# Kernel tuning notes

Measured on AMD Instinct MI355X. Metric: run time of the kernel, lower is better.

The kernel has to match this reference:

```python
import jax, jax.numpy as jnp
import numpy as np

N_CLASSES = 16384
M = 2
D = 128


def setup_inputs() -> dict:
    key = jax.random.key(0)
    k1, k2 = jax.random.split(key)
    x = jax.random.normal(k1, (N_CLASSES * M, D), dtype=jnp.float32)
    anchor_idx = jax.random.randint(k2, (N_CLASSES,), 0, M, dtype=jnp.int64 if jax.config.jax_enable_x64 else jnp.int32).astype(jnp.int32)
    pos_idx = (1 - anchor_idx).astype(jnp.int32)  # randperm(2) -> positive is the other sample
    return {"x": x, "anchor_idx": anchor_idx, "pos_idx": pos_idx}


def reference(x, anchor_idx, pos_idx):
    # x: [N*M, D]; anchor_idx/pos_idx: [N] in [0, M)
    N = anchor_idx.shape[0]
    Dx = x.shape[1]
    xr = x.reshape(N, M, Dx)
    anchors = jnp.take_along_axis(xr, anchor_idx[:, None, None], axis=1)[:, 0, :]    # [N, D]
    positives = jnp.take_along_axis(xr, pos_idx[:, None, None], axis=1)[:, 0, :]     # [N, D]
    negs = xr[:, 1, :]                                                               # [N, D] (sample 1 of every class)
    # score[i, j] = a_i . (neg_j - pos_i) = a_i . neg_j - a_i . pos_i
    S = anchors @ negs.T                                                             # [N, N]
    ap = jnp.sum(anchors * positives, axis=1)                                        # [N]
    logits = S - ap[:, None]
    mask = ~jnp.eye(N, dtype=bool)                                                   # exclude j == i (own class)
    sums = jnp.sum(jnp.where(mask, jnp.exp(logits), jnp.float32(0.0)), axis=1)       # [N]
    return jnp.sum(jnp.log1p(sums))
```

## Files before the change

### kernel.cpp

```cpp
#include <hip/hip_runtime.h>
#include <hip/hip_bf16.h>
#include <math.h>

#define N_CLS 16384
#define DDIM  128
#define LOG2E 1.4426950408889634f

#if __has_builtin(__builtin_amdgcn_exp2f)
#define EXP2(x) __builtin_amdgcn_exp2f(x)
#else
#define EXP2(x) exp2f(x)
#endif

typedef __attribute__((ext_vector_type(8))) short short8;
typedef __attribute__((ext_vector_type(16))) float f32x16;

__device__ __forceinline__ unsigned short f2bf(float f) {
    __hip_bfloat16 h = __float2bfloat16(f);
    return *(unsigned short*)&h;
}

__global__ __launch_bounds__(256)
void prep_kernel(const float* __restrict__ x,
                 const int* __restrict__ aidx,
                 float* __restrict__ ap,
                 unsigned short* __restrict__ Afrag,
                 unsigned short* __restrict__ Bfrag,
                 float* __restrict__ out) {
    const int t = threadIdx.x;
    const int g = blockIdx.x;
    #pragma unroll
    for (int u = 0; u < 4; ++u) {
        const int l  = u * 256 + t;
        const int r  = l >> 4;
        const int k0 = (l & 15) * 8;
        const float* src = x + (long)g * 8192 + (long)r * 128 + k0;
        float fa[8];
        *(float4*)&fa[0] = *(const float4*)(src);
        *(float4*)&fa[4] = *(const float4*)(src + 4);
        const long dst = (long)g * 4096 +
                         ((l & 15) >> 1) * 512 + ((l & 1) * 32 + (r >> 1)) * 8;
        if (r & 1) {
            short8 B;
            #pragma unroll
            for (int j = 0; j < 8; ++j) B[j] = (short)f2bf(fa[j]);
            *(short8*)(Bfrag + dst) = B;
        } else {
            float fb[8];
            *(float4*)&fb[0] = *(const float4*)(src + 128);
            *(float4*)&fb[4] = *(const float4*)(src + 132);
            const int i = g * 32 + (r >> 1);
            const bool sel = (aidx[i] != 0);
            short8 A;
            float d = 0.0f;
            #pragma unroll
            for (int j = 0; j < 8; ++j) {
                const float av = sel ? fb[j] : fa[j];
                A[j] = (short)f2bf(av * LOG2E);
                d += fa[j] * fb[j];
            }
            *(short8*)(Afrag + dst) = A;
            d += __shfl_xor(d, 1, 64);
            d += __shfl_xor(d, 2, 64);
            d += __shfl_xor(d, 4, 64);
            d += __shfl_xor(d, 8, 64);
            if ((t & 15) == 0) ap[i] = d;
        }
    }
    if (t == 0 && g == 0) out[0] = 0.0f;
}

__global__ __launch_bounds__(256, 3)
void fused_kernel(const unsigned short* __restrict__ Afrag,
                  const unsigned short* __restrict__ Bfrag,
                  float* __restrict__ partial) {
    __shared__ __align__(16) unsigned short bs[2][4096];
    const int tid  = threadIdx.x;
    const int lane = tid & 63;
    const int w    = tid >> 6;
    const int l31  = lane & 31;
    const int hi   = lane >> 5;
    const int oct  = blockIdx.x & 7;
    const int rt   = blockIdx.x >> 3;
    const int r0   = rt * 8 + w * 2;
    const int r1   = r0 + 1;

    short8 af0[8], af1[8];
    {
        const unsigned short* a0 = Afrag + (long)r0 * 4096 + lane * 8;
        const unsigned short* a1 = Afrag + (long)r1 * 4096 + lane * 8;
        #pragma unroll
        for (int kc = 0; kc < 8; ++kc) {
            af0[kc] = *(const short8*)(a0 + kc * 512);
            af1[kc] = *(const short8*)(a1 + kc * 512);
        }
    }
    const unsigned short* bbase = Bfrag + (long)oct * (64L * 4096) + lane * 8;
    const int wchunk = w * 1024;

    const int ctd0 = r0 - oct * 64;
    const int ctd1 = r1 - oct * 64;

    float rs0[16], rs1[16];
    #pragma unroll
    for (int q = 0; q < 16; ++q) { rs0[q] = 0.0f; rs1[q] = 0.0f; }

    {
        short8 s0 = *(const short8*)(bbase + wchunk);
        short8 s1 = *(const short8*)(bbase + wchunk + 512);
        *(short8*)(&bs[0][wchunk + lane * 8]) = s0;
        *(short8*)(&bs[0][wchunk + 512 + lane * 8]) = s1;
    }
    __syncthreads();

    for (int ct = 0; ct < 64; ++ct) {
        const int cur = ct & 1;
        const long nt = (ct < 63) ? (long)(ct + 1) : 63L;
        short8 n0 = *(const short8*)(bbase + nt * 4096 + wchunk);
        short8 n1 = *(const short8*)(bbase + nt * 4096 + wchunk + 512);

        f32x16 acc0, acc1;
        #pragma unroll
        for (int q = 0; q < 16; ++q) { acc0[q] = 0.0f; acc1[q] = 0.0f; }

        const unsigned short* bp = &bs[cur][lane * 8];
        #pragma unroll
        for (int kc = 0; kc < 8; ++kc) {
            short8 b = *(const short8*)(bp + kc * 512);
            acc0 = __builtin_amdgcn_mfma_f32_32x32x16_bf16(af0[kc], b, acc0, 0, 0, 0);
            acc1 = __builtin_amdgcn_mfma_f32_32x32x16_bf16(af1[kc], b, acc1, 0, 0, 0);
        }

        if (ct == ctd0) {
            #pragma unroll
            for (int q = 0; q < 16; ++q) {
                const float e = EXP2(acc0[q]);
                const int row = (q & 3) + 8 * (q >> 2) + 4 * hi;
                rs0[q] += (l31 == row) ? 0.0f : e;
            }
        } else {
            #pragma unroll
            for (int q = 0; q < 16; ++q) rs0[q] += EXP2(acc0[q]);
        }
        if (ct == ctd1) {
            #pragma unroll
            for (int q = 0; q < 16; ++q) {
                const float e = EXP2(acc1[q]);
                const int row = (q & 3) + 8 * (q >> 2) + 4 * hi;
                rs1[q] += (l31 == row) ? 0.0f : e;
            }
        } else {
            #pragma unroll
            for (int q = 0; q < 16; ++q) rs1[q] += EXP2(acc1[q]);
        }

        *(short8*)(&bs[cur ^ 1][wchunk + lane * 8]) = n0;
        *(short8*)(&bs[cur ^ 1][wchunk + 512 + lane * 8]) = n1;
        __syncthreads();
    }

    #pragma unroll
    for (int q = 0; q < 16; ++q) {
        float v0 = rs0[q], v1 = rs1[q];
        v0 += __shfl_xor(v0, 1, 64);  v1 += __shfl_xor(v1, 1, 64);
        v0 += __shfl_xor(v0, 2, 64);  v1 += __shfl_xor(v1, 2, 64);
        v0 += __shfl_xor(v0, 4, 64);  v1 += __shfl_xor(v1, 4, 64);
        v0 += __shfl_xor(v0, 8, 64);  v1 += __shfl_xor(v1, 8, 64);
        v0 += __shfl_xor(v0, 16, 64); v1 += __shfl_xor(v1, 16, 64);
        if (l31 == 0) {
            const int row = (q & 3) + 8 * (q >> 2) + 4 * hi;
            partial[(long)oct * N_CLS + (long)r0 * 32 + row] = v0;
            partial[(long)oct * N_CLS + (long)r1 * 32 + row] = v1;
        }
    }
}

__global__ __launch_bounds__(256)
void finalize_kernel(const float* __restrict__ partial,
                     const float* __restrict__ ap,
                     float* __restrict__ out) {
    __shared__ float red[256];
    const int t = threadIdx.x;
    const int row = blockIdx.x * 256 + t;
    float s = 0.0f;
    #pragma unroll
    for (int p = 0; p < 8; ++p) s += partial[(long)p * N_CLS + row];
    const float u = logf(s) - ap[row];
    const float loss = (u > 25.0f) ? u : log1pf(__expf(u));
    red[t] = loss;
    __syncthreads();
    for (int st = 128; st > 0; st >>= 1) {
        if (t < st) red[t] += red[t + st];
        __syncthreads();
    }
    if (t == 0) atomicAdd(out, red[0]);
}

extern "C" void kernel_launch(void* const* d_in, const int* in_sizes, int n_in,
                              void* d_out, int out_size, void* d_ws, size_t ws_size,
                              hipStream_t stream) {
    const float* x    = (const float*)d_in[0];
    const int*   aidx = (const int*)d_in[1];

    char* ws = (char*)d_ws;
    float* ap             = (float*)(ws);
    float* partial        = (float*)(ws + 131072);
    unsigned short* Afrag = (unsigned short*)(ws + 131072 + 1048576);
    unsigned short* Bfrag = (unsigned short*)(ws + 131072 + 1048576 + 4194304);

    prep_kernel<<<N_CLS / 32, 256, 0, stream>>>(x, aidx, ap, Afrag, Bfrag, (float*)d_out);
    fused_kernel<<<512, 256, 0, stream>>>(Afrag, Bfrag, partial);
    finalize_kernel<<<64, 256, 0, stream>>>(partial, ap, (float*)d_out);
}
```

Before: 141.1 us.

## Software-pipeline MFMA and exp epilogue across double accumulator sets

Splits the column-tile loop into compute and epilogue stages with two sets of accumulators, so the exp2/row-sum epilogue of tile t-1 is issued while the MFMAs for tile t run. The goal is to overlap the transcendental VALU work with matrix-core latency instead of serializing them. The extra accumulators raise register pressure, so launch bounds drop from 3 to 2 waves-per-SIMD occupancy, which could reduce latency hiding elsewhere.

```diff
diff --git a/kernel.cpp b/kernel.cpp
--- a/kernel.cpp
+++ b/kernel.cpp
@@ -70,7 +70,7 @@
     if (t == 0 && g == 0) out[0] = 0.0f;
 }
 
-__global__ __launch_bounds__(256, 3)
+__global__ __launch_bounds__(256, 2)
 void fused_kernel(const unsigned short* __restrict__ Afrag,
                   const unsigned short* __restrict__ Bfrag,
                   float* __restrict__ partial) {
@@ -98,12 +98,65 @@
     const unsigned short* bbase = Bfrag + (long)oct * (64L * 4096) + lane * 8;
     const int wchunk = w * 1024;
 
-    const int ctd0 = r0 - oct * 64;
-    const int ctd1 = r1 - oct * 64;
+    int ctd0 = r0 - oct * 64;
+    int ctd1 = r1 - oct * 64;
+    if (ctd0 < 0 || ctd0 >= 64) ctd0 = -1000;
+    if (ctd1 < 0 || ctd1 >= 64) ctd1 = -1000;
 
     float rs0[16], rs1[16];
     #pragma unroll
     for (int q = 0; q < 16; ++q) { rs0[q] = 0.0f; rs1[q] = 0.0f; }
+
+    const f32x16 zacc = {0.0f, 0.0f, 0.0f, 0.0f, 0.0f, 0.0f, 0.0f, 0.0f,
+                         0.0f, 0.0f, 0.0f, 0.0f, 0.0f, 0.0f, 0.0f, 0.0f};
+    f32x16 aA0, aA1, aB0, aB1;
+
+    auto compute = [&](f32x16& c0, f32x16& c1, const unsigned short* bp) {
+        #pragma unroll
+        for (int kc = 0; kc < 8; ++kc) {
+            short8 b = *(const short8*)(bp + kc * 512);
+            c0 = __builtin_amdgcn_mfma_f32_32x32x16_bf16(
+                     af0[kc], b, (kc == 0) ? zacc : c0, 0, 0, 0);
+            c1 = __builtin_amdgcn_mfma_f32_32x32x16_bf16(
+                     af1[kc], b, (kc == 0) ? zacc : c1, 0, 0, 0);
+        }
+    };
+    auto epi = [&](f32x16& p0, f32x16& p1, int pt) {
+        if (pt == ctd0) {
+            #pragma unroll
+            for (int q = 0; q < 16; ++q) {
+                const float e = EXP2(p0[q]);
+                const int row = (q & 3) + 8 * (q >> 2) + 4 * hi;
+                rs0[q] += (l31 == row) ? 0.0f : e;
+            }
+        } else {
+            #pragma unroll
+            for (int q = 0; q < 16; ++q) rs0[q] += EXP2(p0[q]);
+        }
+        if (pt == ctd1) {
+            #pragma unroll
+            for (int q = 0; q < 16; ++q) {
+                const float e = EXP2(p1[q]);
+                const int row = (q & 3) + 8 * (q >> 2) + 4 * hi;
+                rs1[q] += (l31 == row) ? 0.0f : e;
+            }
+        } else {
+            #pragma unroll
+            for (int q = 0; q < 16; ++q) rs1[q] += EXP2(p1[q]);
+        }
+    };
+    auto step = [&](int t, f32x16& c0, f32x16& c1,
+                    f32x16& p0, f32x16& p1, int pt) {
+        const int cur = t & 1;
+        const long nt = (t < 63) ? (long)(t + 1) : 63L;
+        short8 n0 = *(const short8*)(bbase + nt * 4096 + wchunk);
+        short8 n1 = *(const short8*)(bbase + nt * 4096 + wchunk + 512);
+        compute(c0, c1, &bs[cur][lane * 8]);
+        if (pt >= 0) epi(p0, p1, pt);
+        *(short8*)(&bs[cur ^ 1][wchunk + lane * 8]) = n0;
+        *(short8*)(&bs[cur ^ 1][wchunk + 512 + lane * 8]) = n1;
+        __syncthreads();
+    };
 
     {
         short8 s0 = *(const short8*)(bbase + wchunk);
@@ -113,51 +166,11 @@
     }
     __syncthreads();
 
-    for (int ct = 0; ct < 64; ++ct) {
-        const int cur = ct & 1;
-        const long nt = (ct < 63) ? (long)(ct + 1) : 63L;
-        short8 n0 = *(const short8*)(bbase + nt * 4096 + wchunk);
-        short8 n1 = *(const short8*)(bbase + nt * 4096 + wchunk + 512);
-
-        f32x16 acc0, acc1;
-        #pragma unroll
-        for (int q = 0; q < 16; ++q) { acc0[q] = 0.0f; acc1[q] = 0.0f; }
-
-        const unsigned short* bp = &bs[cur][lane * 8];
-        #pragma unroll
-        for (int kc = 0; kc < 8; ++kc) {
-            short8 b = *(const short8*)(bp + kc * 512);
-            acc0 = __builtin_amdgcn_mfma_f32_32x32x16_bf16(af0[kc], b, acc0, 0, 0, 0);
-            acc1 = __builtin_amdgcn_mfma_f32_32x32x16_bf16(af1[kc], b, acc1, 0, 0, 0);
-        }
-
-        if (ct == ctd0) {
-            #pragma unroll
-            for (int q = 0; q < 16; ++q) {
-                const float e = EXP2(acc0[q]);
-                const int row = (q & 3) + 8 * (q >> 2) + 4 * hi;
-                rs0[q] += (l31 == row) ? 0.0f : e;
-            }
-        } else {
-            #pragma unroll
-            for (int q = 0; q < 16; ++q) rs0[q] += EXP2(acc0[q]);
-        }
-        if (ct == ctd1) {
-            #pragma unroll
-            for (int q = 0; q < 16; ++q) {
-                const float e = EXP2(acc1[q]);
-                const int row = (q & 3) + 8 * (q >> 2) + 4 * hi;
-                rs1[q] += (l31 == row) ? 0.0f : e;
-            }
-        } else {
-            #pragma unroll
-            for (int q = 0; q < 16; ++q) rs1[q] += EXP2(acc1[q]);
-        }
-
-        *(short8*)(&bs[cur ^ 1][wchunk + lane * 8]) = n0;
-        *(short8*)(&bs[cur ^ 1][wchunk + 512 + lane * 8]) = n1;
-        __syncthreads();
-    }
+    for (int t = 0; t < 64; t += 2) {
+        step(t,     aA0, aA1, aB0, aB1, t - 1);
+        step(t + 1, aB0, aB1, aA0, aA1, t);
+    }
+    epi(aB0, aB1, 63);
 
     #pragma unroll
     for (int q = 0; q < 16; ++q) {
```

New measurement: 143.8 us. Within noise of the previous version (+1.9%).

## Halve per-wave row tiles in fused kernel, doubling grid and occupancy

Applied to the files above, without the earlier changes.

Each wave of the fused kernel now computes one 32-row anchor tile instead of two. The grid doubles to 1024 blocks and launch bounds rise to 4 blocks per SM, trading B-tile reuse for fewer registers and more parallelism. The MFMA loop is wrapped in s_setprio, and the prep kernel is flattened to one thread per 8-element slice that writes A and B fragments together. The cost is that B is loaded from global and LDS twice as often per unit of work.

```diff
diff --git a/kernel.cpp b/kernel.cpp
--- a/kernel.cpp
+++ b/kernel.cpp
@@ -27,50 +27,42 @@
                  unsigned short* __restrict__ Afrag,
                  unsigned short* __restrict__ Bfrag,
                  float* __restrict__ out) {
-    const int t = threadIdx.x;
-    const int g = blockIdx.x;
+    const int u  = blockIdx.x * 256 + threadIdx.x;
+    const int i  = u >> 4;
+    const int sl = u & 15;
+    const int k0 = sl * 8;
+
+    const float* pa = x + (2L * i) * DDIM + k0;
+    float fa[8], fb[8];
+    *(float4*)&fa[0] = *(const float4*)(pa);
+    *(float4*)&fa[4] = *(const float4*)(pa + 4);
+    *(float4*)&fb[0] = *(const float4*)(pa + DDIM);
+    *(float4*)&fb[4] = *(const float4*)(pa + DDIM + 4);
+    const bool sel = (aidx[i] != 0);
+
+    short8 A, B;
+    float d = 0.0f;
     #pragma unroll
-    for (int u = 0; u < 4; ++u) {
-        const int l  = u * 256 + t;
-        const int r  = l >> 4;
-        const int k0 = (l & 15) * 8;
-        const float* src = x + (long)g * 8192 + (long)r * 128 + k0;
-        float fa[8];
-        *(float4*)&fa[0] = *(const float4*)(src);
-        *(float4*)&fa[4] = *(const float4*)(src + 4);
-        const long dst = (long)g * 4096 +
-                         ((l & 15) >> 1) * 512 + ((l & 1) * 32 + (r >> 1)) * 8;
-        if (r & 1) {
-            short8 B;
-            #pragma unroll
-            for (int j = 0; j < 8; ++j) B[j] = (short)f2bf(fa[j]);
-            *(short8*)(Bfrag + dst) = B;
-        } else {
-            float fb[8];
-            *(float4*)&fb[0] = *(const float4*)(src + 128);
-            *(float4*)&fb[4] = *(const float4*)(src + 132);
-            const int i = g * 32 + (r >> 1);
-            const bool sel = (aidx[i] != 0);
-            short8 A;
-            float d = 0.0f;
-            #pragma unroll
-            for (int j = 0; j < 8; ++j) {
-                const float av = sel ? fb[j] : fa[j];
-                A[j] = (short)f2bf(av * LOG2E);
-                d += fa[j] * fb[j];
-            }
-            *(short8*)(Afrag + dst) = A;
-            d += __shfl_xor(d, 1, 64);
-            d += __shfl_xor(d, 2, 64);
-            d += __shfl_xor(d, 4, 64);
-            d += __shfl_xor(d, 8, 64);
-            if ((t & 15) == 0) ap[i] = d;
-        }
+    for (int j = 0; j < 8; ++j) {
+        const float av = sel ? fb[j] : fa[j];
+        A[j] = (short)f2bf(av * LOG2E);
+        B[j] = (short)f2bf(fb[j]);
+        d += fa[j] * fb[j];
     }
-    if (t == 0 && g == 0) out[0] = 0.0f;
+    const long dst = (long)(i >> 5) * 4096 + (sl >> 1) * 512 +
+                     ((sl & 1) * 32 + (i & 31)) * 8;
+    *(short8*)(Afrag + dst) = A;
+    *(short8*)(Bfrag + dst) = B;
+
+    d += __shfl_xor(d, 1, 64);
+    d += __shfl_xor(d, 2, 64);
+    d += __shfl_xor(d, 4, 64);
+    d += __shfl_xor(d, 8, 64);
+    if (sl == 0) ap[i] = d;
+    if (u == 0) out[0] = 0.0f;
 }
 
-__global__ __launch_bounds__(256, 3)
+__global__ __launch_bounds__(256, 4)
 void fused_kernel(const unsigned short* __restrict__ Afrag,
                   const unsigned short* __restrict__ Bfrag,
                   float* __restrict__ partial) {
@@ -82,28 +74,24 @@
     const int hi   = lane >> 5;
     const int oct  = blockIdx.x & 7;
     const int rt   = blockIdx.x >> 3;
-    const int r0   = rt * 8 + w * 2;
-    const int r1   = r0 + 1;
+    const int gRow = rt * 4 + w;
 
-    short8 af0[8], af1[8];
+    short8 af[8];
     {
-        const unsigned short* a0 = Afrag + (long)r0 * 4096 + lane * 8;
-        const unsigned short* a1 = Afrag + (long)r1 * 4096 + lane * 8;
+        const unsigned short* a0 = Afrag + (long)gRow * 4096 + lane * 8;
         #pragma unroll
-        for (int kc = 0; kc < 8; ++kc) {
-            af0[kc] = *(const short8*)(a0 + kc * 512);
-            af1[kc] = *(const short8*)(a1 + kc * 512);
-        }
+        for (int kc = 0; kc < 8; ++kc)
+            af[kc] = *(const short8*)(a0 + kc * 512);
     }
     const unsigned short* bbase = Bfrag + (long)oct * (64L * 4096) + lane * 8;
     const int wchunk = w * 1024;
 
-    const int ctd0 = r0 - oct * 64;
-    const int ctd1 = r1 - oct * 64;
+    int ctd = gRow - oct * 64;
+    if (ctd < 0 || ctd >= 64) ctd = -1000;
 
-    float rs0[16], rs1[16];
+    float rs[16];
     #pragma unroll
-    for (int q = 0; q < 16; ++q) { rs0[q] = 0.0f; rs1[q] = 0.0f; }
+    for (int q = 0; q < 16; ++q) rs[q] = 0.0f;
 
     {
         short8 s0 = *(const short8*)(bbase + wchunk);
@@ -119,39 +107,29 @@
         short8 n0 = *(const short8*)(bbase + nt * 4096 + wchunk);
         short8 n1 = *(const short8*)(bbase + nt * 4096 + wchunk + 512);
 
-        f32x16 acc0, acc1;
+        f32x16 acc;
         #pragma unroll
-        for (int q = 0; q < 16; ++q) { acc0[q] = 0.0f; acc1[q] = 0.0f; }
+        for (int q = 0; q < 16; ++q) acc[q] = 0.0f;
 
         const unsigned short* bp = &bs[cur][lane * 8];
+        __builtin_amdgcn_s_setprio(1);
         #pragma unroll
         for (int kc = 0; kc < 8; ++kc) {
             short8 b = *(const short8*)(bp + kc * 512);
-            acc0 = __builtin_amdgcn_mfma_f32_32x32x16_bf16(af0[kc], b, acc0, 0, 0, 0);
-            acc1 = __builtin_amdgcn_mfma_f32_32x32x16_bf16(af1[kc], b, acc1, 0, 0, 0);
+            acc = __builtin_amdgcn_mfma_f32_32x32x16_bf16(af[kc], b, acc, 0, 0, 0);
         }
+        __builtin_amdgcn_s_setprio(0);
 
-        if (ct == ctd0) {
+        if (ct == ctd) {
             #pragma unroll
             for (int q = 0; q < 16; ++q) {
-                const float e = EXP2(acc0[q]);
+                const float e = EXP2(acc[q]);
                 const int row = (q & 3) + 8 * (q >> 2) + 4 * hi;
-                rs0[q] += (l31 == row) ? 0.0f : e;
+                rs[q] += (l31 == row) ? 0.0f : e;
             }
         } else {
             #pragma unroll
-            for (int q = 0; q < 16; ++q) rs0[q] += EXP2(acc0[q]);
-        }
-        if (ct == ctd1) {
-            #pragma unroll
-            for (int q = 0; q < 16; ++q) {
-                const float e = EXP2(acc1[q]);
-                const int row = (q & 3) + 8 * (q >> 2) + 4 * hi;
-                rs1[q] += (l31 == row) ? 0.0f : e;
-            }
-        } else {
-            #pragma unroll
-            for (int q = 0; q < 16; ++q) rs1[q] += EXP2(acc1[q]);
+            for (int q = 0; q < 16; ++q) rs[q] += EXP2(acc[q]);
         }
 
         *(short8*)(&bs[cur ^ 1][wchunk + lane * 8]) = n0;
@@ -161,16 +139,15 @@
 
     #pragma unroll
     for (int q = 0; q < 16; ++q) {
-        float v0 = rs0[q], v1 = rs1[q];
-        v0 += __shfl_xor(v0, 1, 64);  v1 += __shfl_xor(v1, 1, 64);
-        v0 += __shfl_xor(v0, 2, 64);  v1 += __shfl_xor(v1, 2, 64);
-        v0 += __shfl_xor(v0, 4, 64);  v1 += __shfl_xor(v1, 4, 64);
-        v0 += __shfl_xor(v0, 8, 64);  v1 += __shfl_xor(v1, 8, 64);
-        v0 += __shfl_xor(v0, 16, 64); v1 += __shfl_xor(v1, 16, 64);
+        float v = rs[q];
+        v += __shfl_xor(v, 1, 64);
+        v += __shfl_xor(v, 2, 64);
+        v += __shfl_xor(v, 4, 64);
+        v += __shfl_xor(v, 8, 64);
+        v += __shfl_xor(v, 16, 64);
         if (l31 == 0) {
             const int row = (q & 3) + 8 * (q >> 2) + 4 * hi;
-            partial[(long)oct * N_CLS + (long)r0 * 32 + row] = v0;
-            partial[(long)oct * N_CLS + (long)r1 * 32 + row] = v1;
+            partial[(long)oct * N_CLS + (long)gRow * 32 + row] = v;
         }
     }
 }
@@ -208,7 +185,7 @@
     unsigned short* Afrag = (unsigned short*)(ws + 131072 + 1048576);
     unsigned short* Bfrag = (unsigned short*)(ws + 131072 + 1048576 + 4194304);
 
-    prep_kernel<<<N_CLS / 32, 256, 0, stream>>>(x, aidx, ap, Afrag, Bfrag, (float*)d_out);
-    fused_kernel<<<512, 256, 0, stream>>>(Afrag, Bfrag, partial);
+    prep_kernel<<<1024, 256, 0, stream>>>(x, aidx, ap, Afrag, Bfrag, (float*)d_out);
+    fused_kernel<<<1024, 256, 0, stream>>>(Afrag, Bfrag, partial);
     finalize_kernel<<<64, 256, 0, stream>>>(partial, ap, (float*)d_out);
 }
```

Result: slower. 143.9 us (+2.0%).

## Split column range into 16 groups, simplify prep, raise MFMA priority

Applied to the files above, without the earlier changes.

The fused kernel now splits the negative columns into 16 groups of 32 tiles instead of 8 groups of 64, launching 1024 blocks instead of 512. This gives more parallelism and better load balance across the CUs, at the cost of twice as many partial sums for finalize to read and twice the A-fragment reloads. The prep kernel is rewritten so each thread handles one 8-element slice of both samples of a class, producing the A and B fragments together. The MFMA loop is also wrapped in s_setprio to favour the matrix issue.

```diff
diff --git a/kernel.cpp b/kernel.cpp
--- a/kernel.cpp
+++ b/kernel.cpp
@@ -27,47 +27,39 @@
                  unsigned short* __restrict__ Afrag,
                  unsigned short* __restrict__ Bfrag,
                  float* __restrict__ out) {
-    const int t = threadIdx.x;
-    const int g = blockIdx.x;
-    #pragma unroll
-    for (int u = 0; u < 4; ++u) {
-        const int l  = u * 256 + t;
-        const int r  = l >> 4;
-        const int k0 = (l & 15) * 8;
-        const float* src = x + (long)g * 8192 + (long)r * 128 + k0;
-        float fa[8];
-        *(float4*)&fa[0] = *(const float4*)(src);
-        *(float4*)&fa[4] = *(const float4*)(src + 4);
-        const long dst = (long)g * 4096 +
-                         ((l & 15) >> 1) * 512 + ((l & 1) * 32 + (r >> 1)) * 8;
-        if (r & 1) {
-            short8 B;
-            #pragma unroll
-            for (int j = 0; j < 8; ++j) B[j] = (short)f2bf(fa[j]);
-            *(short8*)(Bfrag + dst) = B;
-        } else {
-            float fb[8];
-            *(float4*)&fb[0] = *(const float4*)(src + 128);
-            *(float4*)&fb[4] = *(const float4*)(src + 132);
-            const int i = g * 32 + (r >> 1);
-            const bool sel = (aidx[i] != 0);
-            short8 A;
-            float d = 0.0f;
-            #pragma unroll
-            for (int j = 0; j < 8; ++j) {
-                const float av = sel ? fb[j] : fa[j];
-                A[j] = (short)f2bf(av * LOG2E);
-                d += fa[j] * fb[j];
-            }
-            *(short8*)(Afrag + dst) = A;
-            d += __shfl_xor(d, 1, 64);
-            d += __shfl_xor(d, 2, 64);
-            d += __shfl_xor(d, 4, 64);
-            d += __shfl_xor(d, 8, 64);
-            if ((t & 15) == 0) ap[i] = d;
-        }
-    }
-    if (t == 0 && g == 0) out[0] = 0.0f;
+    const int u  = blockIdx.x * 256 + threadIdx.x;
+    const int i  = u >> 4;
+    const int sl = u & 15;
+    const int k0 = sl * 8;
+
+    const float* pa = x + (2L * i) * DDIM + k0;
+    float fa[8], fb[8];
+    *(float4*)&fa[0] = *(const float4*)(pa);
+    *(float4*)&fa[4] = *(const float4*)(pa + 4);
+    *(float4*)&fb[0] = *(const float4*)(pa + DDIM);
+    *(float4*)&fb[4] = *(const float4*)(pa + DDIM + 4);
+    const bool sel = (aidx[i] != 0);
+
+    short8 A, B;
+    float d = 0.0f;
+    #pragma unroll
+    for (int j = 0; j < 8; ++j) {
+        const float av = sel ? fb[j] : fa[j];
+        A[j] = (short)f2bf(av * LOG2E);
+        B[j] = (short)f2bf(fb[j]);
+        d += fa[j] * fb[j];
+    }
+    const long dst = (long)(i >> 5) * 4096 + (sl >> 1) * 512 +
+                     ((sl & 1) * 32 + (i & 31)) * 8;
+    *(short8*)(Afrag + dst) = A;
+    *(short8*)(Bfrag + dst) = B;
+
+    d += __shfl_xor(d, 1, 64);
+    d += __shfl_xor(d, 2, 64);
+    d += __shfl_xor(d, 4, 64);
+    d += __shfl_xor(d, 8, 64);
+    if (sl == 0) ap[i] = d;
+    if (u == 0) out[0] = 0.0f;
 }
 
 __global__ __launch_bounds__(256, 3)
@@ -80,8 +72,8 @@
     const int w    = tid >> 6;
     const int l31  = lane & 31;
     const int hi   = lane >> 5;
-    const int oct  = blockIdx.x & 7;
-    const int rt   = blockIdx.x >> 3;
+    const int cg   = blockIdx.x & 15;
+    const int rt   = blockIdx.x >> 4;
     const int r0   = rt * 8 + w * 2;
     const int r1   = r0 + 1;
 
@@ -95,11 +87,13 @@
             af1[kc] = *(const short8*)(a1 + kc * 512);
         }
     }
-    const unsigned short* bbase = Bfrag + (long)oct * (64L * 4096) + lane * 8;
+    const unsigned short* bbase = Bfrag + (long)cg * (32L * 4096) + lane * 8;
     const int wchunk = w * 1024;
 
-    const int ctd0 = r0 - oct * 64;
-    const int ctd1 = r1 - oct * 64;
+    int ctd0 = r0 - cg * 32;
+    int ctd1 = r1 - cg * 32;
+    if (ctd0 < 0 || ctd0 >= 32) ctd0 = -1000;
+    if (ctd1 < 0 || ctd1 >= 32) ctd1 = -1000;
 
     float rs0[16], rs1[16];
     #pragma unroll
@@ -113,9 +107,9 @@
     }
     __syncthreads();
 
-    for (int ct = 0; ct < 64; ++ct) {
+    for (int ct = 0; ct < 32; ++ct) {
         const int cur = ct & 1;
-        const long nt = (ct < 63) ? (long)(ct + 1) : 63L;
+        const long nt = (ct < 31) ? (long)(ct + 1) : 31L;
         short8 n0 = *(const short8*)(bbase + nt * 4096 + wchunk);
         short8 n1 = *(const short8*)(bbase + nt * 4096 + wchunk + 512);
 
@@ -124,12 +118,14 @@
         for (int q = 0; q < 16; ++q) { acc0[q] = 0.0f; acc1[q] = 0.0f; }
 
         const unsigned short* bp = &bs[cur][lane * 8];
+        __builtin_amdgcn_s_setprio(1);
         #pragma unroll
         for (int kc = 0; kc < 8; ++kc) {
             short8 b = *(const short8*)(bp + kc * 512);
             acc0 = __builtin_amdgcn_mfma_f32_32x32x16_bf16(af0[kc], b, acc0, 0, 0, 0);
             acc1 = __builtin_amdgcn_mfma_f32_32x32x16_bf16(af1[kc], b, acc1, 0, 0, 0);
         }
+        __builtin_amdgcn_s_setprio(0);
 
         if (ct == ctd0) {
             #pragma unroll
@@ -169,8 +165,8 @@
         v0 += __shfl_xor(v0, 16, 64); v1 += __shfl_xor(v1, 16, 64);
         if (l31 == 0) {
             const int row = (q & 3) + 8 * (q >> 2) + 4 * hi;
-            partial[(long)oct * N_CLS + (long)r0 * 32 + row] = v0;
-            partial[(long)oct * N_CLS + (long)r1 * 32 + row] = v1;
+            partial[(long)cg * N_CLS + (long)r0 * 32 + row] = v0;
+            partial[(long)cg * N_CLS + (long)r1 * 32 + row] = v1;
         }
     }
 }
@@ -184,7 +180,7 @@
     const int row = blockIdx.x * 256 + t;
     float s = 0.0f;
     #pragma unroll
-    for (int p = 0; p < 8; ++p) s += partial[(long)p * N_CLS + row];
+    for (int p = 0; p < 16; ++p) s += partial[(long)p * N_CLS + row];
     const float u = logf(s) - ap[row];
     const float loss = (u > 25.0f) ? u : log1pf(__expf(u));
     red[t] = loss;
@@ -208,7 +204,7 @@
     unsigned short* Afrag = (unsigned short*)(ws + 131072 + 1048576);
     unsigned short* Bfrag = (unsigned short*)(ws + 131072 + 1048576 + 4194304);
 
-    prep_kernel<<<N_CLS / 32, 256, 0, stream>>>(x, aidx, ap, Afrag, Bfrag, (float*)d_out);
-    fused_kernel<<<512, 256, 0, stream>>>(Afrag, Bfrag, partial);
+    prep_kernel<<<1024, 256, 0, stream>>>(x, aidx, ap, Afrag, Bfrag, (float*)d_out);
+    fused_kernel<<<1024, 256, 0, stream>>>(Afrag, Bfrag, partial);
     finalize_kernel<<<64, 256, 0, stream>>>(partial, ap, (float*)d_out);
 }
```

New measurement: 144.8 us. +2.6%, slower.
